# Performance work log

Hardware: AMD Instinct MI355X
Metric: run time of the kernel (lower is better)

## Reference

```python
import jax, jax.numpy as jnp
import numpy as np

TEMPERATURE = 0.5

def setup_inputs() -> dict:
    key = jax.random.key(0)
    k1, k2 = jax.random.split(key)
    N, D = 4096, 128
    emb_i = jax.random.normal(k1, (N, D), dtype=jnp.float32)
    emb_j = jax.random.normal(k2, (N, D), dtype=jnp.float32)
    return {"emb_i": emb_i, "emb_j": emb_j}

def reference(emb_i, emb_j):
    # L2-normalize each embedding (F.normalize, dim=1)
    z_i = emb_i / jnp.linalg.norm(emb_i, axis=1, keepdims=True)
    z_j = emb_j / jnp.linalg.norm(emb_j, axis=1, keepdims=True)
    N = z_j.shape[0]
    reps = jnp.concatenate([z_i, z_j], axis=0)  # [2N, D], unit rows
    # cosine similarity of unit vectors == dot product
    logits = jnp.einsum('id,jd->ij', reps, reps) / TEMPERATURE  # [2N, 2N]
    # denominator excludes only k == i (self), positive pair included
    diag_mask = jnp.eye(2 * N, dtype=bool)
    masked = jnp.where(diag_mask, -jnp.inf, logits)
    lse = jax.nn.logsumexp(masked, axis=1)  # [2N]
    # positive index: i <-> i+N
    pos_idx = jnp.concatenate([jnp.arange(N) + N, jnp.arange(N)])
    pos_logits = jnp.take_along_axis(logits, pos_idx[:, None], axis=1)[:, 0]
    # loss = mean over all 2N anchors of -(log numerator - log denominator)
    loss = jnp.mean(lse - pos_logits)
    return loss
```

## Files before the change

kernel.cpp:

```cpp
#include <hip/hip_runtime.h>
#include <hip/hip_bf16.h>

#define NROW 4096
#define D 128
#define TOT 8192
#define PRESCALE 1.69864407f
#define GRID_G 1024
#define CPB 256
#define NT 16

typedef __attribute__((ext_vector_type(8))) short bf16x8;
typedef __attribute__((ext_vector_type(4))) float f32x4;

__device__ __forceinline__ float fast_exp2(float x) {
#if __has_builtin(__builtin_amdgcn_exp2f)
  return __builtin_amdgcn_exp2f(x);
#else
  return exp2f(x);
#endif
}
__device__ __forceinline__ float fast_log2(float x) {
#if __has_builtin(__builtin_amdgcn_logf)
  return __builtin_amdgcn_logf(x);
#else
  return log2f(x);
#endif
}

__device__ __forceinline__ unsigned short f2bf(float x) {
  unsigned u = __float_as_uint(x);
  unsigned r = (u + 0x7fffu + ((u >> 16) & 1u)) >> 16;
  return (unsigned short)r;
}

__device__ __forceinline__ void gload16(const void* g, void* l) {
  __builtin_amdgcn_global_load_lds(
      (const __attribute__((address_space(1))) unsigned int*)g,
      (__attribute__((address_space(3))) unsigned int*)l, 16, 0, 0);
}

__global__ __launch_bounds__(256) void k_norm(
    const float* __restrict__ ei, const float* __restrict__ ej,
    unsigned short* __restrict__ Zp, float* __restrict__ pos,
    float* __restrict__ rowsum, unsigned* __restrict__ ctr) {
  int gid = blockIdx.x * 256 + (int)threadIdx.x;
  if (gid < TOT) rowsum[gid] = 0.0f;
  if (gid == TOT) *ctr = 0u;

  int wid = threadIdx.x >> 6;
  int lane = threadIdx.x & 63;
  int r = blockIdx.x * 4 + wid;
  const float2 xi = *(const float2*)(ei + (size_t)r * D + lane * 2);
  const float2 xj = *(const float2*)(ej + (size_t)r * D + lane * 2);
  float si = xi.x * xi.x + xi.y * xi.y;
  float sj = xj.x * xj.x + xj.y * xj.y;
  float dd = xi.x * xj.x + xi.y * xj.y;
#pragma unroll
  for (int m = 32; m >= 1; m >>= 1) {
    si += __shfl_xor(si, m, 64);
    sj += __shfl_xor(sj, m, 64);
    dd += __shfl_xor(dd, m, 64);
  }
  float ri = rsqrtf(si); ri = ri * (1.5f - 0.5f * si * ri * ri);
  float rj = rsqrtf(sj); rj = rj * (1.5f - 0.5f * sj * rj * rj);
  unsigned short a0 = f2bf(xi.x * ri * PRESCALE);
  unsigned short a1 = f2bf(xi.y * ri * PRESCALE);
  unsigned short b0 = f2bf(xj.x * rj * PRESCALE);
  unsigned short b1 = f2bf(xj.y * rj * PRESCALE);
  ((unsigned*)(Zp + (size_t)r * D))[lane] = (unsigned)a0 | ((unsigned)a1 << 16);
  ((unsigned*)(Zp + (size_t)(r + NROW) * D))[lane] = (unsigned)b0 | ((unsigned)b1 << 16);
  if (lane == 0) pos[r] = 2.0f * dd * ri * rj;
}

__global__ __launch_bounds__(256, 4) void k_gemm(
    const unsigned short* __restrict__ Zp, float* __restrict__ rowsum,
    const float* __restrict__ pos, unsigned* __restrict__ ctr,
    float* __restrict__ out) {
  __shared__ __align__(16) char ldsb[8192];
  const int tid = (int)threadIdx.x;
  const int wid = tid >> 6, lane = tid & 63;
  const int lo = lane & 15, hi = lane >> 4;
  const unsigned b = blockIdx.x;
  const int cs = (int)((b & 7u) * 4u + ((b >> 3) & 3u));
  const int rb = (int)(b >> 5);
  const int rowbase = rb * 256 + wid * 64;

  bf16x8 af[4][4];
#pragma unroll
  for (int g = 0; g < 4; ++g) {
    const unsigned short* za = Zp + (size_t)(rowbase + g * 16 + lo) * D + hi * 8;
#pragma unroll
    for (int kk = 0; kk < 4; ++kk) af[g][kk] = *(const bf16x8*)(za + kk * 32);
  }

  int rdoff[4];
  const int sw = (lo & 7) << 4;
#pragma unroll
  for (int kk = 0; kk < 4; ++kk) rdoff[kk] = lo * 256 + (((kk * 4 + hi) * 16) ^ sw);

  const int Rr = wid * 4 + (lane >> 4);
  const int B0 = (lane & 15) * 16;
  const char* gbase = (const char*)Zp + (size_t)cs * CPB * 256 +
                      (size_t)Rr * 256 + (size_t)(B0 ^ ((Rr & 7) << 4));
  char* ldsw = ldsb + wid * 1024;

  float sums[4][4];
#pragma unroll
  for (int g = 0; g < 4; ++g)
#pragma unroll
    for (int r = 0; r < 4; ++r) sums[g][r] = 0.0f;

  const bool blkdiag = (cs == rb);

  gload16(gbase, ldsw);
  asm volatile("s_waitcnt vmcnt(0)" ::: "memory");

#pragma unroll 2
  for (int t = 0; t < NT; ++t) {
    if (t + 1 < NT) {
      gload16(gbase + (size_t)(t + 1) * 4096, ldsw + ((t + 1) & 1) * 4096);
      asm volatile("s_waitcnt vmcnt(1)" ::: "memory");
    } else {
      asm volatile("s_waitcnt vmcnt(0)" ::: "memory");
    }
    __builtin_amdgcn_s_barrier();

    const char* ldsr = ldsb + (t & 1) * 4096;
    f32x4 acc[4];
#pragma unroll
    for (int g = 0; g < 4; ++g) acc[g] = (f32x4){0.f, 0.f, 0.f, 0.f};
#pragma unroll
    for (int kk = 0; kk < 4; ++kk) {
      bf16x8 bfv = *(const bf16x8*)(ldsr + rdoff[kk]);
#pragma unroll
      for (int g = 0; g < 4; ++g)
        acc[g] = __builtin_amdgcn_mfma_f32_16x16x32_bf16(af[g][kk], bfv, acc[g], 0, 0, 0);
    }
    const int gd = blkdiag ? (t - wid * 4) : -1;
#pragma unroll
    for (int g = 0; g < 4; ++g)
#pragma unroll
      for (int r = 0; r < 4; ++r) {
        float e = fast_exp2(acc[g][r]);
        sums[g][r] += (g == gd && lo == hi * 4 + r) ? 0.0f : e;
      }
    asm volatile("s_waitcnt lgkmcnt(0)" ::: "memory");
    __builtin_amdgcn_sched_barrier(0);
    __builtin_amdgcn_s_barrier();
  }

#pragma unroll
  for (int g = 0; g < 4; ++g)
#pragma unroll
    for (int r = 0; r < 4; ++r) {
      float v = sums[g][r];
      v += __shfl_xor(v, 1, 64);
      v += __shfl_xor(v, 2, 64);
      v += __shfl_xor(v, 4, 64);
      v += __shfl_xor(v, 8, 64);
      if (lo == 0) atomicAdd(&rowsum[rowbase + g * 16 + hi * 4 + r], v);
    }

  __syncthreads();
  __shared__ unsigned slast;
  if (tid == 0) {
    __threadfence();
    slast = atomicAdd(ctr, 1u);
  }
  __syncthreads();
  if (slast == GRID_G - 1) {
    float s1 = 0.0f, s2 = 0.0f;
    for (int k = tid; k < TOT; k += 256) {
      float v = __hip_atomic_load(&rowsum[k], __ATOMIC_RELAXED, __HIP_MEMORY_SCOPE_AGENT);
      s1 += fast_log2(v);
    }
    for (int k = tid; k < NROW; k += 256) s2 += pos[k];
    float c = s1 * (0.69314718055994531f / (float)TOT) - s2 * (1.0f / (float)NROW);
#pragma unroll
    for (int m = 32; m >= 1; m >>= 1) c += __shfl_xor(c, m, 64);
    __shared__ float wsum[4];
    if (lane == 0) wsum[wid] = c;
    __syncthreads();
    if (tid == 0) out[0] = wsum[0] + wsum[1] + wsum[2] + wsum[3];
  }
}

extern "C" void kernel_launch(void* const* d_in, const int* in_sizes, int n_in,
                              void* d_out, int out_size, void* d_ws, size_t ws_size,
                              hipStream_t stream) {
  const float* ei = (const float*)d_in[0];
  const float* ej = (const float*)d_in[1];
  float* out = (float*)d_out;
  float* rowsum = (float*)d_ws;
  float* pos = (float*)((char*)d_ws + TOT * 4);
  unsigned* ctr = (unsigned*)((char*)d_ws + TOT * 4 + NROW * 4);
  unsigned short* Zp =
      (unsigned short*)((char*)d_ws + TOT * 4 + NROW * 4 + 256);

  k_norm<<<NROW / 4, 256, 0, stream>>>(ei, ej, Zp, pos, rowsum, ctr);
  k_gemm<<<GRID_G, 256, 0, stream>>>(Zp, rowsum, pos, ctr, out);
}
```

Measured before the change: 108.5 us.

## Stage B tiles in 64-row phases with larger LDS buffers and fewer barriers

The GEMM loop now loads four 16-row column subtiles per phase, 16 KB per buffer, and runs four phases instead of sixteen single-subtile steps. That cuts per-iteration barriers and waitcnt stalls from sixteen to four and issues four async global-to-LDS loads per wave per phase. MFMA sections are wrapped in s_setprio, and the diagonal-mask test now uses a global row-tile index with a full 16-way XOR swizzle. LDS use rises from 8 KB to 32 KB per block, which may limit occupancy at four blocks per CU.

Measured after the change: 243.7 us. 2.25x slower.

```diff
diff --git a/kernel.cpp b/kernel.cpp
--- a/kernel.cpp
+++ b/kernel.cpp
@@ -5,35 +5,24 @@
 #define D 128
 #define TOT 8192
 #define PRESCALE 1.69864407f
+#define LN2 0.69314718055994531f
 #define GRID_G 1024
-#define CPB 256
-#define NT 16
+#define NP 4
 
 typedef __attribute__((ext_vector_type(8))) short bf16x8;
 typedef __attribute__((ext_vector_type(4))) float f32x4;
 
-__device__ __forceinline__ float fast_exp2(float x) {
-#if __has_builtin(__builtin_amdgcn_exp2f)
+static __device__ __forceinline__ float fast_exp2(float x) {
   return __builtin_amdgcn_exp2f(x);
-#else
-  return exp2f(x);
-#endif
-}
-__device__ __forceinline__ float fast_log2(float x) {
-#if __has_builtin(__builtin_amdgcn_logf)
+}
+static __device__ __forceinline__ float fast_log2(float x) {
   return __builtin_amdgcn_logf(x);
-#else
-  return log2f(x);
-#endif
-}
-
-__device__ __forceinline__ unsigned short f2bf(float x) {
+}
+static __device__ __forceinline__ unsigned short f2bf(float x) {
   unsigned u = __float_as_uint(x);
-  unsigned r = (u + 0x7fffu + ((u >> 16) & 1u)) >> 16;
-  return (unsigned short)r;
-}
-
-__device__ __forceinline__ void gload16(const void* g, void* l) {
+  return (unsigned short)((u + 0x7fffu + ((u >> 16) & 1u)) >> 16);
+}
+static __device__ __forceinline__ void gload16(const void* g, void* l) {
   __builtin_amdgcn_global_load_lds(
       (const __attribute__((address_space(1))) unsigned int*)g,
       (__attribute__((address_space(3))) unsigned int*)l, 16, 0, 0);
@@ -63,12 +52,10 @@
   }
   float ri = rsqrtf(si); ri = ri * (1.5f - 0.5f * si * ri * ri);
   float rj = rsqrtf(sj); rj = rj * (1.5f - 0.5f * sj * rj * rj);
-  unsigned short a0 = f2bf(xi.x * ri * PRESCALE);
-  unsigned short a1 = f2bf(xi.y * ri * PRESCALE);
-  unsigned short b0 = f2bf(xj.x * rj * PRESCALE);
-  unsigned short b1 = f2bf(xj.y * rj * PRESCALE);
-  ((unsigned*)(Zp + (size_t)r * D))[lane] = (unsigned)a0 | ((unsigned)a1 << 16);
-  ((unsigned*)(Zp + (size_t)(r + NROW) * D))[lane] = (unsigned)b0 | ((unsigned)b1 << 16);
+  ((unsigned*)(Zp + (size_t)r * D))[lane] =
+      (unsigned)f2bf(xi.x * ri * PRESCALE) | ((unsigned)f2bf(xi.y * ri * PRESCALE) << 16);
+  ((unsigned*)(Zp + (size_t)(r + NROW) * D))[lane] =
+      (unsigned)f2bf(xj.x * rj * PRESCALE) | ((unsigned)f2bf(xj.y * rj * PRESCALE) << 16);
   if (lane == 0) pos[r] = 2.0f * dd * ri * rj;
 }
 
@@ -76,14 +63,15 @@
     const unsigned short* __restrict__ Zp, float* __restrict__ rowsum,
     const float* __restrict__ pos, unsigned* __restrict__ ctr,
     float* __restrict__ out) {
-  __shared__ __align__(16) char ldsb[8192];
+  __shared__ __align__(16) char ldsb[32768];
   const int tid = (int)threadIdx.x;
   const int wid = tid >> 6, lane = tid & 63;
   const int lo = lane & 15, hi = lane >> 4;
-  const unsigned b = blockIdx.x;
-  const int cs = (int)((b & 7u) * 4u + ((b >> 3) & 3u));
-  const int rb = (int)(b >> 5);
+  const int b = (int)blockIdx.x;
+  const int cs = (b & 7) * 4 + ((b >> 3) & 3);
+  const int rb = b >> 5;
   const int rowbase = rb * 256 + wid * 64;
+  const int RT0 = rb * 16 + wid * 4;
 
   bf16x8 af[4][4];
 #pragma unroll
@@ -93,16 +81,17 @@
     for (int kk = 0; kk < 4; ++kk) af[g][kk] = *(const bf16x8*)(za + kk * 32);
   }
 
-  int rdoff[4];
-  const int sw = (lo & 7) << 4;
-#pragma unroll
-  for (int kk = 0; kk < 4; ++kk) rdoff[kk] = lo * 256 + (((kk * 4 + hi) * 16) ^ sw);
-
-  const int Rr = wid * 4 + (lane >> 4);
-  const int B0 = (lane & 15) * 16;
-  const char* gbase = (const char*)Zp + (size_t)cs * CPB * 256 +
-                      (size_t)Rr * 256 + (size_t)(B0 ^ ((Rr & 7) << 4));
-  char* ldsw = ldsb + wid * 1024;
+  const char* zb = (const char*)Zp + (size_t)cs * 65536;
+  int goff[4];
+#pragma unroll
+  for (int q = 0; q < 4; ++q) {
+    int row = wid * 16 + q * 4 + hi;
+    goff[q] = row * 256 + ((lo * 16) ^ ((row & 15) << 4));
+  }
+  int rdo[4];
+#pragma unroll
+  for (int kk = 0; kk < 4; ++kk)
+    rdo[kk] = lo * 256 + (((kk * 4 + hi) * 16) ^ (lo << 4));
 
   float sums[4][4];
 #pragma unroll
@@ -110,44 +99,53 @@
 #pragma unroll
     for (int r = 0; r < 4; ++r) sums[g][r] = 0.0f;
 
-  const bool blkdiag = (cs == rb);
-
-  gload16(gbase, ldsw);
+#define STAGE(pp, buf)                                                \
+  do {                                                                \
+    char* ld_ = ldsb + (buf) * 16384 + wid * 4096;                    \
+    const char* gp_ = zb + (size_t)(pp) * 16384;                      \
+    gload16(gp_ + goff[0], ld_);                                      \
+    gload16(gp_ + goff[1], ld_ + 1024);                               \
+    gload16(gp_ + goff[2], ld_ + 2048);                               \
+    gload16(gp_ + goff[3], ld_ + 3072);                               \
+  } while (0)
+
+  STAGE(0, 0);
   asm volatile("s_waitcnt vmcnt(0)" ::: "memory");
-
-#pragma unroll 2
-  for (int t = 0; t < NT; ++t) {
-    if (t + 1 < NT) {
-      gload16(gbase + (size_t)(t + 1) * 4096, ldsw + ((t + 1) & 1) * 4096);
-      asm volatile("s_waitcnt vmcnt(1)" ::: "memory");
-    } else {
-      asm volatile("s_waitcnt vmcnt(0)" ::: "memory");
+  __builtin_amdgcn_s_barrier();
+
+#pragma unroll
+  for (int p = 0; p < NP; ++p) {
+    const int cur = p & 1;
+    if (p + 1 < NP) STAGE(p + 1, cur ^ 1);
+#pragma unroll
+    for (int st = 0; st < 4; ++st) {
+      const char* sb = ldsb + cur * 16384 + st * 4096;
+      f32x4 acc[4];
+#pragma unroll
+      for (int g = 0; g < 4; ++g) acc[g] = (f32x4){0.f, 0.f, 0.f, 0.f};
+      __builtin_amdgcn_s_setprio(1);
+#pragma unroll
+      for (int kk = 0; kk < 4; ++kk) {
+        bf16x8 bv = *(const bf16x8*)(sb + rdo[kk]);
+#pragma unroll
+        for (int g = 0; g < 4; ++g)
+          acc[g] = __builtin_amdgcn_mfma_f32_16x16x32_bf16(af[g][kk], bv, acc[g], 0, 0, 0);
+      }
+      __builtin_amdgcn_s_setprio(0);
+      const int gd = cs * 16 + p * 4 + st - RT0;
+#pragma unroll
+      for (int g = 0; g < 4; ++g)
+#pragma unroll
+        for (int r = 0; r < 4; ++r) {
+          float e = fast_exp2(acc[g][r]);
+          if (g == gd && lo == hi * 4 + r) e = 0.0f;
+          sums[g][r] += e;
+        }
     }
+    asm volatile("s_waitcnt vmcnt(0)" ::: "memory");
     __builtin_amdgcn_s_barrier();
-
-    const char* ldsr = ldsb + (t & 1) * 4096;
-    f32x4 acc[4];
-#pragma unroll
-    for (int g = 0; g < 4; ++g) acc[g] = (f32x4){0.f, 0.f, 0.f, 0.f};
-#pragma unroll
-    for (int kk = 0; kk < 4; ++kk) {
-      bf16x8 bfv = *(const bf16x8*)(ldsr + rdoff[kk]);
-#pragma unroll
-      for (int g = 0; g < 4; ++g)
-        acc[g] = __builtin_amdgcn_mfma_f32_16x16x32_bf16(af[g][kk], bfv, acc[g], 0, 0, 0);
-    }
-    const int gd = blkdiag ? (t - wid * 4) : -1;
-#pragma unroll
-    for (int g = 0; g < 4; ++g)
-#pragma unroll
-      for (int r = 0; r < 4; ++r) {
-        float e = fast_exp2(acc[g][r]);
-        sums[g][r] += (g == gd && lo == hi * 4 + r) ? 0.0f : e;
-      }
-    asm volatile("s_waitcnt lgkmcnt(0)" ::: "memory");
-    __builtin_amdgcn_sched_barrier(0);
-    __builtin_amdgcn_s_barrier();
-  }
+  }
+#undef STAGE
 
 #pragma unroll
   for (int g = 0; g < 4; ++g)
@@ -169,19 +167,19 @@
   }
   __syncthreads();
   if (slast == GRID_G - 1) {
+    __threadfence();
     float s1 = 0.0f, s2 = 0.0f;
-    for (int k = tid; k < TOT; k += 256) {
-      float v = __hip_atomic_load(&rowsum[k], __ATOMIC_RELAXED, __HIP_MEMORY_SCOPE_AGENT);
-      s1 += fast_log2(v);
-    }
+    for (int k = tid; k < TOT; k += 256)
+      s1 += fast_log2(__hip_atomic_load(&rowsum[k], __ATOMIC_RELAXED,
+                                        __HIP_MEMORY_SCOPE_AGENT));
     for (int k = tid; k < NROW; k += 256) s2 += pos[k];
-    float c = s1 * (0.69314718055994531f / (float)TOT) - s2 * (1.0f / (float)NROW);
+    float c = s1 * (LN2 / (float)TOT) - s2 * (1.0f / (float)NROW);
 #pragma unroll
     for (int m = 32; m >= 1; m >>= 1) c += __shfl_xor(c, m, 64);
-    __shared__ float wsum[4];
-    if (lane == 0) wsum[wid] = c;
+    __shared__ float ws4[4];
+    if (lane == 0) ws4[wid] = c;
     __syncthreads();
-    if (tid == 0) out[0] = wsum[0] + wsum[1] + wsum[2] + wsum[3];
+    if (tid == 0) out[0] = ws4[0] + ws4[1] + ws4[2] + ws4[3];
   }
 }
 
```
